# Performance work log

Hardware: AMD Instinct MI355X
Metric: run time of the kernel (lower is better)

Reference implementation:

```python
import jax, jax.numpy as jnp
import numpy as np

N_NODES = 50000
N_EDGES = 800000
NODE_DIM = 64
HIDDEN = 128
OUT_DIM = 256
N_LAYERS = 3


def setup_inputs() -> dict:
    key = jax.random.key(0)
    ks = jax.random.split(key, 12)
    inp = {
        'x': jax.random.normal(ks[0], (N_NODES, NODE_DIM), dtype=jnp.float32),
        'src': jax.random.randint(ks[1], (N_EDGES,), 0, N_NODES, dtype=jnp.int32),
        'dst': jax.random.randint(ks[2], (N_EDGES,), 0, N_NODES, dtype=jnp.int32),
        'Wp': jax.random.normal(ks[3], (NODE_DIM, HIDDEN), dtype=jnp.float32) / np.sqrt(NODE_DIM),
        'bp': jax.random.normal(ks[4], (HIDDEN,), dtype=jnp.float32) * 0.01,
        'Wg': jax.random.normal(ks[5], (N_LAYERS, HIDDEN, HIDDEN), dtype=jnp.float32) / np.sqrt(HIDDEN),
        'bg': jax.random.normal(ks[6], (N_LAYERS, HIDDEN), dtype=jnp.float32) * 0.01,
        'W1': jax.random.normal(ks[7], (HIDDEN, HIDDEN), dtype=jnp.float32) / np.sqrt(HIDDEN),
        'b1': jax.random.normal(ks[8], (HIDDEN,), dtype=jnp.float32) * 0.01,
        'W2': jax.random.normal(ks[9], (HIDDEN, OUT_DIM), dtype=jnp.float32) / np.sqrt(HIDDEN),
        'b2': jax.random.normal(ks[10], (OUT_DIM,), dtype=jnp.float32) * 0.01,
    }
    return inp


def reference(x, src, dst, Wp, bp, Wg, bg, W1, b1, W2, b2):
    n = x.shape[0]
    # node_proj
    h = x @ Wp + bp  # [N, H]
    # in-degree per dst node; zero-degree nodes keep a zero message
    deg = jax.ops.segment_sum(jnp.ones_like(src, dtype=h.dtype), dst, num_segments=n)  # [N]
    inv_deg = jnp.where(deg > 0, 1.0 / jnp.maximum(deg, 1.0), 0.0)[:, None]  # [N,1]
    for l in range(Wg.shape[0]):
        # gather neighbor embeddings along edges, mean-aggregate into dst
        msg = jax.ops.segment_sum(h[src], dst, num_segments=n) * inv_deg  # [N, H]
        h = jax.nn.relu(h + msg @ Wg[l] + bg[l])
    g = jnp.mean(h, axis=0)  # [H]
    latent = jax.nn.relu(g @ W1 + b1) @ W2 + b2  # [OUT_DIM]
    return latent
```

## Files before the change

kernel.cpp:

```cpp
#include <hip/hip_runtime.h>
#include <hip/hip_fp16.h>

#define H   128
#define ND  64
#define TILE_R 64
#define CAP 64
#define NSCAT 2048

typedef _Float16 f16x8 __attribute__((ext_vector_type(8)));
typedef float    f32x4 __attribute__((ext_vector_type(4)));

__device__ __forceinline__ unsigned short f2h(float f) {
  return __half_as_ushort(__float2half(f));
}
__device__ __forceinline__ float h2f(unsigned short u) {
  return __half2float(__ushort_as_half(u));
}


__global__ __launch_bounds__(256) void prep_all_k(const float* __restrict__ Wg,
                                                  const float* __restrict__ Wp,
                                                  unsigned short* __restrict__ wfrag,
                                                  unsigned short* __restrict__ wpfrag,
                                                  int* __restrict__ cnt, int n_pad,
                                                  float* __restrict__ gsum,
                                                  int* __restrict__ done) {
  __shared__ float sW[H * H];
  if (blockIdx.x < 3) {
    const float* W = Wg + (size_t)blockIdx.x * H * H;
    for (int i = threadIdx.x; i < H * H; i += 256) sW[i] = W[i];
    __syncthreads();
    unsigned short* out = wfrag + (size_t)blockIdx.x * 2048 * 8;
    for (int c = threadIdx.x; c < 2048; c += 256) {
      int lane = c & 63, combo = c >> 6;
      int it = combo >> 2, ks = combo & 3;
      int nc = it * 16 + (lane & 15);
      int kb = ks * 32 + (lane >> 4) * 8;
      unsigned short* o = out + (size_t)c * 8;
#pragma unroll
      for (int j = 0; j < 8; ++j) o[j] = f2h(sW[(kb + j) * H + nc]);
    }
  } else if (blockIdx.x == 3) {
    for (int i = threadIdx.x; i < ND * H; i += 256) sW[i] = Wp[i];
    __syncthreads();
    for (int c = threadIdx.x; c < 1024; c += 256) {
      int lane = c & 63, combo = c >> 6;
      int it = combo >> 1, ks = combo & 1;
      int nc = it * 16 + (lane & 15);
      int kb = ks * 32 + (lane >> 4) * 8;
      unsigned short* o = wpfrag + (size_t)c * 8;
#pragma unroll
      for (int j = 0; j < 8; ++j) o[j] = f2h(sW[(kb + j) * H + nc]);
    }
  } else {
    int zb = blockIdx.x - 4;
    int chunk = (n_pad + 15) >> 4;
    int lo = zb * chunk, hi = lo + chunk; if (hi > n_pad) hi = n_pad;
    for (int i = lo + threadIdx.x; i < hi; i += 256) cnt[i] = 0;
    if (zb == 0) {
      if (threadIdx.x < H) gsum[threadIdx.x] = 0.f;
      if (threadIdx.x == 0) *done = 0;
    }
  }
}


__global__ __launch_bounds__(256) void scatter_proj_k(
    const int* __restrict__ src, const int* __restrict__ dst,
    int* __restrict__ cnt, unsigned short* __restrict__ ssrc, int E, int psz,
    const float* __restrict__ x, const unsigned short* __restrict__ wpfrag,
    const float* __restrict__ bp, unsigned short* __restrict__ hout, int n) {
  __shared__ unsigned short sB[1024 * 8];
  if ((int)blockIdx.x < NSCAT) {
    int grp = blockIdx.x & 7;
    int lo = grp * psz, hi = lo + psz;
    int stride = (NSCAT >> 3) * 256;
    for (int e = ((int)blockIdx.x >> 3) * 256 + (int)threadIdx.x; e < E; e += stride) {
      int d = dst[e];
      if (d >= lo && d < hi) {
        int p = atomicAdd(&cnt[d], 1);
        if (p < CAP) ssrc[(size_t)d * CAP + p] = (unsigned short)src[e];
      }
    }
    return;
  }

  uint4* sB4 = (uint4*)sB;
  const uint4* wsrc = (const uint4*)wpfrag;
  for (int i = threadIdx.x; i < 1024; i += 256) sB4[i] = wsrc[i];
  __syncthreads();

  int wave = threadIdx.x >> 6, lane = threadIdx.x & 63;
  int quad = lane >> 4, n16 = lane & 15;
  int node = ((int)blockIdx.x - NSCAT) * 64 + wave * 16 + n16;

  union { unsigned short s[8]; uint4 u; f16x8 h; } bm[2];
  if (node < n) {
    const float* xr = x + (size_t)node * ND;
#pragma unroll
    for (int ks = 0; ks < 2; ++ks) {
      const float* pk = xr + ks * 32 + quad * 8;
      float4 A0 = *(const float4*)pk;
      float4 A1 = *(const float4*)(pk + 4);
      bm[ks].s[0] = f2h(A0.x); bm[ks].s[1] = f2h(A0.y);
      bm[ks].s[2] = f2h(A0.z); bm[ks].s[3] = f2h(A0.w);
      bm[ks].s[4] = f2h(A1.x); bm[ks].s[5] = f2h(A1.y);
      bm[ks].s[6] = f2h(A1.z); bm[ks].s[7] = f2h(A1.w);
    }
  } else {
    bm[0].u = make_uint4(0, 0, 0, 0);
    bm[1].u = make_uint4(0, 0, 0, 0);
  }

  f32x4 acc[8] = {};
#pragma unroll
  for (int it = 0; it < 8; ++it) {
#pragma unroll
    for (int ks = 0; ks < 2; ++ks) {
      union { uint4 u; f16x8 h; } aw;
      aw.u = sB4[(it * 2 + ks) * 64 + lane];
      acc[it] = __builtin_amdgcn_mfma_f32_16x16x32_f16(aw.h, bm[ks].h, acc[it], 0, 0, 0);
    }
  }

  unsigned short* rout = hout + (size_t)node * H;
#pragma unroll
  for (int it = 0; it < 8; ++it) {
    int f0 = it * 16 + quad * 4;
    float4 bv = *(const float4*)(bp + f0);
    ushort4 o = make_ushort4(f2h(acc[it][0] + bv.x), f2h(acc[it][1] + bv.y),
                             f2h(acc[it][2] + bv.z), f2h(acc[it][3] + bv.w));
    *(ushort4*)(rout + f0) = o;
  }
}


__global__ __launch_bounds__(256) void aggregate_w_k(
    const unsigned short* __restrict__ hin,
    const int* __restrict__ cnt,
    const unsigned short* __restrict__ ssrc,
    unsigned short* __restrict__ msgh, int n) {
  int node = blockIdx.x * 4 + (threadIdx.x >> 6);
  if (node >= n) return;
  int l = threadIdx.x & 63;
  int sub = l >> 4, li = l & 15;
  int deg = cnt[node]; if (deg > CAP) deg = CAP;
  const __half2 z = __floats2half2_rn(0.f, 0.f);
  __half2 acc[4] = {z, z, z, z};
  if (deg > 0) {
    int eid = (int)ssrc[(size_t)node * CAP + (l < deg ? l : 0)];
    int j = 0;
#pragma unroll 4
    for (; j + 4 <= deg; j += 4) {
      int s = __shfl(eid, j + sub, 64);
      union { uint4 u; __half2 h[4]; } v;
      v.u = *(const uint4*)(hin + (size_t)s * H + li * 8);
      acc[0] = __hadd2(acc[0], v.h[0]);
      acc[1] = __hadd2(acc[1], v.h[1]);
      acc[2] = __hadd2(acc[2], v.h[2]);
      acc[3] = __hadd2(acc[3], v.h[3]);
    }
    if (j < deg) {
      int jj = j + sub;
      int s = __shfl(eid, jj < deg ? jj : deg - 1, 64);
      if (jj < deg) {
        union { uint4 u; __half2 h[4]; } v;
        v.u = *(const uint4*)(hin + (size_t)s * H + li * 8);
        acc[0] = __hadd2(acc[0], v.h[0]);
        acc[1] = __hadd2(acc[1], v.h[1]);
        acc[2] = __hadd2(acc[2], v.h[2]);
        acc[3] = __hadd2(acc[3], v.h[3]);
      }
    }
  }
#pragma unroll
  for (int k = 0; k < 4; ++k) {
    union { __half2 h; unsigned int u; } a, b, c;
    a.h = acc[k];
    b.u = __shfl_xor(a.u, 16, 64);
    a.h = __hadd2(a.h, b.h);
    c.u = __shfl_xor(a.u, 32, 64);
    acc[k] = __hadd2(a.h, c.h);
  }
  if (sub == 0) {
    float inv = (deg > 0) ? 1.0f / (float)deg : 0.f;
    uint4 o;
    unsigned int* op = (unsigned int*)&o;
#pragma unroll
    for (int k = 0; k < 4; ++k) {
      float lo = __low2float(acc[k]) * inv;
      float hi = __high2float(acc[k]) * inv;
      op[k] = (unsigned int)f2h(lo) | ((unsigned int)f2h(hi) << 16);
    }
    *(uint4*)(msgh + (size_t)node * H + li * 8) = o;
  }
}


__global__ __launch_bounds__(256, 4) void update_mfma_k(
    const unsigned short* __restrict__ hin,
    unsigned short* __restrict__ hout,
    const unsigned short* __restrict__ msgh,
    const unsigned short* __restrict__ wfrag,
    const float* __restrict__ bg, int n) {
  __shared__ unsigned short sB[2048 * 8];
  uint4* sB4 = (uint4*)sB;
  const uint4* wsrc = (const uint4*)wfrag;
  for (int i = threadIdx.x; i < 2048; i += 256) sB4[i] = wsrc[i];
  __syncthreads();

  int wave = threadIdx.x >> 6, lane = threadIdx.x & 63;
  int quad = lane >> 4, n16 = lane & 15;
  int node = blockIdx.x * 64 + wave * 16 + n16;

  union { uint4 u; f16x8 h; } bm[4];
  const unsigned short* mrow = msgh + (size_t)node * H;
#pragma unroll
  for (int ks = 0; ks < 4; ++ks)
    bm[ks].u = *(const uint4*)(mrow + ks * 32 + quad * 8);

  f32x4 acc[8] = {};
#pragma unroll
  for (int it = 0; it < 8; ++it) {
#pragma unroll
    for (int ks = 0; ks < 4; ++ks) {
      union { uint4 u; f16x8 h; } aw;
      aw.u = sB4[(it * 4 + ks) * 64 + lane];
      acc[it] = __builtin_amdgcn_mfma_f32_16x16x32_f16(aw.h, bm[ks].h, acc[it], 0, 0, 0);
    }
  }

  const unsigned short* rin = hin + (size_t)node * H;
  unsigned short* rout = hout + (size_t)node * H;
#pragma unroll
  for (int it = 0; it < 8; ++it) {
    int f0 = it * 16 + quad * 4;
    float4 bv = *(const float4*)(bg + f0);
    ushort4 old = *(const ushort4*)(rin + f0);
    float v0 = h2f(old.x) + acc[it][0] + bv.x; v0 = v0 > 0.f ? v0 : 0.f;
    float v1 = h2f(old.y) + acc[it][1] + bv.y; v1 = v1 > 0.f ? v1 : 0.f;
    float v2 = h2f(old.z) + acc[it][2] + bv.z; v2 = v2 > 0.f ? v2 : 0.f;
    float v3 = h2f(old.w) + acc[it][3] + bv.w; v3 = v3 > 0.f ? v3 : 0.f;
    *(ushort4*)(rout + f0) = make_ushort4(f2h(v0), f2h(v1), f2h(v2), f2h(v3));
  }
}


__global__ __launch_bounds__(256) void pool_mlp_k(
    const unsigned short* __restrict__ hb, float* __restrict__ gsum,
    int* __restrict__ done,
    const float* __restrict__ W1, const float* __restrict__ b1,
    const float* __restrict__ W2, const float* __restrict__ b2,
    float* __restrict__ out, float invN, int n, int nblocks) {
  int c  = threadIdx.x & 31;
  int rg = threadIdx.x >> 5;
  float4 acc = {0.f, 0.f, 0.f, 0.f};
#pragma unroll 4
  for (int row = blockIdx.x * 8 + rg; row < n; row += gridDim.x * 8) {
    ushort4 v = ((const ushort4*)(hb + (size_t)row * H))[c];
    acc.x += h2f(v.x); acc.y += h2f(v.y);
    acc.z += h2f(v.z); acc.w += h2f(v.w);
  }
  __shared__ float4 s[256];
  s[threadIdx.x] = acc;
  __syncthreads();
  if (threadIdx.x < 32) {
    float4 t = s[c];
#pragma unroll
    for (int k = 1; k < 8; ++k) {
      float4 q = s[k * 32 + c];
      t.x += q.x; t.y += q.y; t.z += q.z; t.w += q.w;
    }
    atomicAdd(&gsum[c * 4 + 0], t.x);
    atomicAdd(&gsum[c * 4 + 1], t.y);
    atomicAdd(&gsum[c * 4 + 2], t.z);
    atomicAdd(&gsum[c * 4 + 3], t.w);
  }
  __threadfence();
  __syncthreads();
  __shared__ int lastflag;
  if (threadIdx.x == 0)
    lastflag = (atomicAdd(done, 1) == nblocks - 1) ? 1 : 0;
  __syncthreads();
  if (!lastflag) return;

  __shared__ float g[H];
  __shared__ float hid[H];
  __shared__ float hpart[256];
  int tid = threadIdx.x;
  if (tid < H) g[tid] = atomicAdd(&gsum[tid], 0.0f) * invN;
  __syncthreads();
  {
    int o = tid & 127, half = tid >> 7;
    int k0 = half * 64;
    float p0 = 0.f, p1 = 0.f, p2 = 0.f, p3 = 0.f;
#pragma unroll
    for (int k = 0; k < 64; k += 4) {
      p0 += g[k0 + k + 0] * W1[(k0 + k + 0) * H + o];
      p1 += g[k0 + k + 1] * W1[(k0 + k + 1) * H + o];
      p2 += g[k0 + k + 2] * W1[(k0 + k + 2) * H + o];
      p3 += g[k0 + k + 3] * W1[(k0 + k + 3) * H + o];
    }
    hpart[tid] = (p0 + p1) + (p2 + p3);
  }
  __syncthreads();
  if (tid < H) {
    float v = hpart[tid] + hpart[tid + 128] + b1[tid];
    hid[tid] = v > 0.f ? v : 0.f;
  }
  __syncthreads();
  {
    float q0 = 0.f, q1 = 0.f, q2 = 0.f, q3 = 0.f;
#pragma unroll
    for (int k = 0; k < H; k += 4) {
      q0 += hid[k + 0] * W2[(k + 0) * 256 + tid];
      q1 += hid[k + 1] * W2[(k + 1) * 256 + tid];
      q2 += hid[k + 2] * W2[(k + 2) * 256 + tid];
      q3 += hid[k + 3] * W2[(k + 3) * 256 + tid];
    }
    out[tid] = b2[tid] + (q0 + q1) + (q2 + q3);
  }
}


extern "C" void kernel_launch(void* const* d_in, const int* in_sizes, int n_in,
                              void* d_out, int out_size, void* d_ws, size_t ws_size,
                              hipStream_t stream) {
  const float* x  = (const float*)d_in[0];
  const int*   src = (const int*)d_in[1];
  const int*   dst = (const int*)d_in[2];
  const float* Wp = (const float*)d_in[3];
  const float* bp = (const float*)d_in[4];
  const float* Wg = (const float*)d_in[5];
  const float* bg = (const float*)d_in[6];
  const float* W1 = (const float*)d_in[7];
  const float* b1 = (const float*)d_in[8];
  const float* W2 = (const float*)d_in[9];
  const float* b2 = (const float*)d_in[10];
  float* out = (float*)d_out;

  const int N = in_sizes[0] / ND;
  const int E = in_sizes[1];
  const int N_pad = ((N + TILE_R - 1) / TILE_R) * TILE_R;
  const size_t NH = (size_t)N_pad * H;
  const int psz = (N_pad + 7) / 8;

  char* p = (char*)d_ws;
  unsigned short* hb0   = (unsigned short*)p; p += NH * sizeof(unsigned short);
  unsigned short* hb1   = (unsigned short*)p; p += NH * sizeof(unsigned short);
  unsigned short* msgh  = (unsigned short*)p; p += NH * sizeof(unsigned short);
  unsigned short* wfrag = (unsigned short*)p; p += 3 * 2048 * 8 * sizeof(unsigned short);
  unsigned short* wpfrag= (unsigned short*)p; p += 1024 * 8 * sizeof(unsigned short);
  unsigned short* ssrc  = (unsigned short*)p; p += (size_t)N_pad * CAP * sizeof(unsigned short);
  int*   cnt  = (int*)p;   p += (size_t)N_pad * sizeof(int);
  float* gsum = (float*)p; p += H * sizeof(float);
  int*   done = (int*)p;   p += sizeof(int);

  const int ntiles = N_pad / TILE_R;
  const int POOLB = 256;

  prep_all_k<<<20, 256, 0, stream>>>(Wg, Wp, wfrag, wpfrag, cnt, N_pad, gsum, done);

  scatter_proj_k<<<NSCAT + ntiles, 256, 0, stream>>>(src, dst, cnt, ssrc, E, psz,
                                                     x, wpfrag, bp, hb0, N);

  unsigned short* hin = hb0;
  unsigned short* hout = hb1;
  for (int l = 0; l < 3; ++l) {
    aggregate_w_k<<<(N + 3) / 4, 256, 0, stream>>>(hin, cnt, ssrc, msgh, N);
    update_mfma_k<<<ntiles, 256, 0, stream>>>(hin, hout, msgh,
                                              wfrag + (size_t)l * 2048 * 8,
                                              bg + (size_t)l * H, N);
    unsigned short* t = hin; hin = hout; hout = t;
  }

  pool_mlp_k<<<POOLB, 256, 0, stream>>>(hin, gsum, done, W1, b1, W2, b2, out,
                                        1.0f / (float)N, N, POOLB);
}
```

Before: 292.9 us.

## Partition edge scatter by hardware XCD with dynamic per-XCD chunk queues

```diff
diff --git a/kernel.cpp b/kernel.cpp
--- a/kernel.cpp
+++ b/kernel.cpp
@@ -6,6 +6,7 @@
 #define TILE_R 64
 #define CAP 64
 #define NSCAT 2048
+#define ECHUNK 4096
 
 typedef _Float16 f16x8 __attribute__((ext_vector_type(8)));
 typedef float    f32x4 __attribute__((ext_vector_type(4)));
@@ -24,7 +25,8 @@
                                                   unsigned short* __restrict__ wpfrag,
                                                   int* __restrict__ cnt, int n_pad,
                                                   float* __restrict__ gsum,
-                                                  int* __restrict__ done) {
+                                                  int* __restrict__ done,
+                                                  int* __restrict__ xcur) {
   __shared__ float sW[H * H];
   if (blockIdx.x < 3) {
     const float* W = Wg + (size_t)blockIdx.x * H * H;
@@ -60,6 +62,7 @@
     if (zb == 0) {
       if (threadIdx.x < H) gsum[threadIdx.x] = 0.f;
       if (threadIdx.x == 0) *done = 0;
+      if (threadIdx.x < 8 * 32) xcur[threadIdx.x] = 0;
     }
   }
 }
@@ -67,19 +70,31 @@
 
 __global__ __launch_bounds__(256) void scatter_proj_k(
     const int* __restrict__ src, const int* __restrict__ dst,
-    int* __restrict__ cnt, unsigned short* __restrict__ ssrc, int E, int psz,
+    int* __restrict__ cnt, unsigned short* __restrict__ ssrc,
+    int* __restrict__ xcur, int E, int psz,
     const float* __restrict__ x, const unsigned short* __restrict__ wpfrag,
     const float* __restrict__ bp, unsigned short* __restrict__ hout, int n) {
   __shared__ unsigned short sB[1024 * 8];
   if ((int)blockIdx.x < NSCAT) {
-    int grp = blockIdx.x & 7;
-    int lo = grp * psz, hi = lo + psz;
-    int stride = (NSCAT >> 3) * 256;
-    for (int e = ((int)blockIdx.x >> 3) * 256 + (int)threadIdx.x; e < E; e += stride) {
-      int d = dst[e];
-      if (d >= lo && d < hi) {
-        int p = atomicAdd(&cnt[d], 1);
-        if (p < CAP) ssrc[(size_t)d * CAP + p] = (unsigned short)src[e];
+    __shared__ int sChunk;
+    unsigned int xcd;
+    asm volatile("s_getreg_b32 %0, hwreg(HW_REG_XCC_ID)" : "=s"(xcd));
+    xcd &= 7;
+    int lo = (int)xcd * psz, hi = lo + psz;
+    int* mycur = xcur + (int)xcd * 32;
+    for (;;) {
+      if (threadIdx.x == 0) sChunk = atomicAdd(mycur, 1);
+      __syncthreads();
+      int e0 = sChunk * ECHUNK;
+      __syncthreads();
+      if (e0 >= E) break;
+      int eend = e0 + ECHUNK; if (eend > E) eend = E;
+      for (int e = e0 + (int)threadIdx.x; e < eend; e += 256) {
+        int d = dst[e];
+        if (d >= lo && d < hi) {
+          int p = atomicAdd(&cnt[d], 1);
+          if (p < CAP) ssrc[(size_t)d * CAP + p] = (unsigned short)src[e];
+        }
       }
     }
     return;
@@ -355,14 +370,17 @@
   int*   cnt  = (int*)p;   p += (size_t)N_pad * sizeof(int);
   float* gsum = (float*)p; p += H * sizeof(float);
   int*   done = (int*)p;   p += sizeof(int);
+  p = (char*)(((uintptr_t)p + 127) & ~(uintptr_t)127);
+  int*   xcur = (int*)p;   p += 8 * 32 * sizeof(int);
 
   const int ntiles = N_pad / TILE_R;
   const int POOLB = 256;
 
-  prep_all_k<<<20, 256, 0, stream>>>(Wg, Wp, wfrag, wpfrag, cnt, N_pad, gsum, done);
-
-  scatter_proj_k<<<NSCAT + ntiles, 256, 0, stream>>>(src, dst, cnt, ssrc, E, psz,
-                                                     x, wpfrag, bp, hb0, N);
+  prep_all_k<<<20, 256, 0, stream>>>(Wg, Wp, wfrag, wpfrag, cnt, N_pad, gsum,
+                                     done, xcur);
+
+  scatter_proj_k<<<NSCAT + ntiles, 256, 0, stream>>>(src, dst, cnt, ssrc, xcur,
+                                                     E, psz, x, wpfrag, bp, hb0, N);
 
   unsigned short* hin = hb0;
   unsigned short* hout = hb1;
```

After: 303.5 us. 1.04x slower.
